# Kernel optimization log

Measured on AMD Instinct MI355X. Metric: run time of the kernel, lower is better.

Reference implementation:

```python
import jax, jax.numpy as jnp
import numpy as np

N_PL = 16      # PiecewiseLin resolution
OBJECTS = 10   # top-k objects kept / max count


def plin(w, x):
    """PiecewiseLin forward: w is [N_PL+1], x is any-shape tensor in [0,1]."""
    w = jnp.abs(w)
    w = w / w.sum()
    csum = jnp.cumsum(w)                     # [N_PL+1]
    y = N_PL * x
    idx = y.astype(jnp.int32)                # trunc toward zero (x >= 0)
    f = y - jnp.trunc(y)                     # fractional part
    lo = csum[jnp.minimum(idx, N_PL)]
    hi = w[jnp.minimum(idx + 1, N_PL)]
    return lo + f * hi


def _area(box):  # box: [n, 4, o]
    return jnp.clip(box[:, 2] - box[:, 0], 0.0, None) * jnp.clip(box[:, 3] - box[:, 1], 0.0, None)


def _iou(a, b):  # a, b: [n, 4, o] -> [n, o, o]
    mn = jnp.maximum(a[:, :2, :, None], b[:, :2, None, :])
    mx = jnp.minimum(a[:, 2:, :, None], b[:, 2:, None, :])
    wh = jnp.clip(mx - mn, 0.0, None)
    inter = wh[:, 0] * wh[:, 1]
    aa = _area(a)[:, :, None]
    ab = _area(b)[:, None, :]
    return inter / (aa + ab - inter + 1e-12)


def counter_forward(boxes, attention, ws):
    n = boxes.shape[0]
    # filter_most_important: top-k by attention
    att, idx = jax.lax.top_k(attention, OBJECTS)                       # [n, o]
    idx_b = jnp.broadcast_to(idx[:, None, :], (n, 4, OBJECTS))
    boxes = jnp.take_along_axis(boxes, idx_b, axis=2)                  # [n, 4, o]
    att = jax.nn.sigmoid(att)                                          # already_sigmoided=False

    relev = att[:, :, None] * att[:, None, :]                          # [n, o, o]
    dist = 1.0 - _iou(boxes, boxes)                                    # [n, o, o]

    score = plin(ws[0], relev) * plin(ws[1], dist)
    dedup = plin(ws[3], relev) * plin(ws[4], dist)

    # deduplicate
    att_diff = jnp.abs(att[:, :, None] - att[:, None, :])              # [n, o, o]
    score_diff = jnp.abs(dedup[..., :, None] - dedup[..., None, :])    # [n, o, o, o]
    sim = plin(ws[2], 1.0 - score_diff).prod(axis=1) * plin(ws[2], 1.0 - att_diff)  # [n, o, o]
    row_sims = sim.sum(axis=2)                                         # [n, o]
    all_sims = row_sims[:, :, None] * row_sims[:, None, :]             # [n, o, o]

    score = score / all_sims
    correction = plin(ws[0], att * att) / row_sims                     # [n, o]
    total = score.sum(axis=(1, 2))[:, None] + correction.sum(axis=1, keepdims=True)  # [n, 1]
    total = jnp.sqrt(total + 1e-20)

    # to_one_hot
    s = jnp.clip(total, 0.0, float(OBJECTS))                           # [n, 1]
    i = s.astype(jnp.int32)[:, 0]
    f = s - jnp.trunc(s)
    tl = jax.nn.one_hot(jnp.minimum(i, OBJECTS), OBJECTS + 1, dtype=s.dtype)
    tr = jax.nn.one_hot(jnp.minimum(i + 1, OBJECTS), OBJECTS + 1, dtype=s.dtype)
    one_hot = (1.0 - f) * tl + f * tr                                  # [n, o+1]

    # confidence
    att_conf = jnp.abs(plin(ws[5], att) - 0.5)                         # [n, o]
    dist_conf = jnp.abs(plin(ws[6], dist) - 0.5)                       # [n, o, o]
    conf = plin(ws[7], att_conf.mean(axis=1, keepdims=True)
                + dist_conf.mean(axis=2).mean(axis=1, keepdims=True))  # [n, 1]
    return one_hot * conf                                              # [n, o+1]


def setup_inputs() -> dict:
    key = jax.random.key(0)
    k1, k2, k3 = jax.random.split(key, 3)
    n, m = 32768, 36
    boxes = jax.random.uniform(k1, (n, 4, m), dtype=jnp.float32)
    attention = jax.random.normal(k2, (n, m), dtype=jnp.float32)
    ws = jax.random.uniform(k3, (8, N_PL + 1), dtype=jnp.float32, minval=0.1, maxval=1.0)
    return {"boxes": boxes, "attention": attention, "ws": ws}


def reference(boxes, attention, ws):
    return counter_forward(boxes, attention, ws)
```

## Files before the change

kernel.cpp:

```cpp
#include <hip/hip_runtime.h>
#include <math.h>

#define N_PL 16
#define NT   17
#define OBJ  10
#define M    36
#define SPB  4
#define BLK  64

#define R_ATT  0
#define R_X0   10
#define R_Y0   20
#define R_X1   30
#define R_Y1   40
#define R_AR   50
#define R_DED  60
#define R_SIM  160
#define R_RF   260
#define RSTRIDE 273

__constant__ unsigned char c_p55[55] = {
 0x00,0x01,0x02,0x03,0x04,0x05,0x06,0x07,0x08,0x09,
 0x11,0x12,0x13,0x14,0x15,0x16,0x17,0x18,0x19,
 0x22,0x23,0x24,0x25,0x26,0x27,0x28,0x29,
 0x33,0x34,0x35,0x36,0x37,0x38,0x39,
 0x44,0x45,0x46,0x47,0x48,0x49,
 0x55,0x56,0x57,0x58,0x59,
 0x66,0x67,0x68,0x69,
 0x77,0x78,0x79,
 0x88,0x89,
 0x99};
__constant__ unsigned char c_p45[45] = {
 0x01,0x02,0x03,0x04,0x05,0x06,0x07,0x08,0x09,
 0x12,0x13,0x14,0x15,0x16,0x17,0x18,0x19,
 0x23,0x24,0x25,0x26,0x27,0x28,0x29,
 0x34,0x35,0x36,0x37,0x38,0x39,
 0x45,0x46,0x47,0x48,0x49,
 0x56,0x57,0x58,0x59,
 0x67,0x68,0x69,
 0x78,0x79,
 0x89};

__device__ __forceinline__ float plin_tab(const float* s_tab, int t, float x) {
    const float* wn = s_tab + t * NT;
    const float* cs = s_tab + 136 + t * NT;
    float y = 16.0f * x;
    int idx = (int)y;
    float f = y - (float)idx;
    int i0 = idx < N_PL ? idx : N_PL;
    int i1 = (idx + 1) < N_PL ? (idx + 1) : N_PL;
    return __builtin_fmaf(f, wn[i1], cs[i0]);
}

__device__ __forceinline__ unsigned long long mkkey(float v, int m) {
    unsigned int b = __float_as_uint(v);
    unsigned int u = b ^ (0x80000000u | (unsigned int)((int)b >> 31));
    return ((unsigned long long)u << 6) | (unsigned int)(63 - m);
}

__global__ __launch_bounds__(BLK, 4) void counter_kernel(
    const float* __restrict__ boxes,
    const float* __restrict__ attn,
    const float* __restrict__ ws,
    float* __restrict__ out,
    int n)
{
    __shared__ float s_tab[272];
    __shared__ float s_reg[SPB * RSTRIDE];

    const int tid = threadIdx.x;
    const int g = tid & 15;
    const int p = tid >> 4;
    float* R = s_reg + p * RSTRIDE;

    if (tid < 8) {
        float w[NT]; float sum = 0.f;
        #pragma unroll
        for (int k = 0; k < NT; ++k) { w[k] = fabsf(ws[tid * NT + k]); sum += w[k]; }
        float rs = 1.f / sum;
        float c = 0.f;
        #pragma unroll
        for (int k = 0; k < NT; ++k) {
            float v = w[k] * rs;
            s_tab[tid * NT + k] = v;
            c += v;
            s_tab[136 + tid * NT + k] = c;
        }
    }

    int s = blockIdx.x * SPB + p;
    const bool active = (s < n);
    if (!active) s = n - 1;

    const float* arow = attn + (size_t)s * M;
    float mv[3]; unsigned long long myk[3];
    #pragma unroll
    for (int k = 0; k < 3; ++k) {
        int e = g + 16 * k;
        bool ok = e < M;
        float v = ok ? arow[e] : 0.f;
        mv[k] = v;
        myk[k] = ok ? mkkey(v, e) : 0ull;
    }
    int rnk0 = 0, rnk1 = 0, rnk2 = 0;
    #pragma unroll
    for (int c4 = 0; c4 < 9; ++c4) {
        float4 t4 = ((const float4*)arow)[c4];
        float vv[4] = {t4.x, t4.y, t4.z, t4.w};
        #pragma unroll
        for (int q = 0; q < 4; ++q) {
            unsigned long long kk = mkkey(vv[q], 4 * c4 + q);
            rnk0 += (kk > myk[0]) ? 1 : 0;
            rnk1 += (kk > myk[1]) ? 1 : 0;
            rnk2 += (kk > myk[2]) ? 1 : 0;
        }
    }
    int rnk[3] = {rnk0, rnk1, rnk2};

    __syncthreads();

    const float* brow = boxes + (size_t)s * (4 * M);
    float mA = 0.f;
    #pragma unroll
    for (int k = 0; k < 3; ++k) {
        int e = g + 16 * k;
        if (e < M && rnk[k] < OBJ) {
            float a = 1.f / (1.f + __expf(-mv[k]));
            int r = rnk[k];
            R[R_ATT + r] = a;
            mA += fabsf(plin_tab(s_tab, 5, a) - 0.5f);
            float x0 = brow[e], y0 = brow[M + e], x1 = brow[2 * M + e], y1 = brow[3 * M + e];
            R[R_X0 + r] = x0; R[R_Y0 + r] = y0;
            R[R_X1 + r] = x1; R[R_Y1 + r] = y1;
            R[R_AR + r] = fmaxf(x1 - x0, 0.f) * fmaxf(y1 - y0, 0.f);
        }
    }
    __syncthreads();

    float mD = 0.f;
    float sc_loc[4];
    #pragma unroll
    for (int t = 0; t < 4; ++t) {
        int q = g + 16 * t;
        bool act = (q < 55);
        int pk = c_p55[act ? q : 0];
        int i = pk >> 4, j = pk & 15;
        float wx = fminf(R[R_X1 + i], R[R_X1 + j]) - fmaxf(R[R_X0 + i], R[R_X0 + j]);
        float wy = fminf(R[R_Y1 + i], R[R_Y1 + j]) - fmaxf(R[R_Y0 + i], R[R_Y0 + j]);
        float inter = fmaxf(wx, 0.f) * fmaxf(wy, 0.f);
        float un = R[R_AR + i] + R[R_AR + j] - inter + 1e-12f;
        float d = 1.f - inter * __builtin_amdgcn_rcpf(un);
        float relev = R[R_ATT + i] * R[R_ATT + j];
        float dd = plin_tab(s_tab, 3, relev) * plin_tab(s_tab, 4, d);
        sc_loc[t] = plin_tab(s_tab, 0, relev) * plin_tab(s_tab, 1, d);
        float dc = fabsf(plin_tab(s_tab, 6, d) - 0.5f);
        if (act) {
            R[R_DED + i * OBJ + j] = dd;
            R[R_DED + j * OBJ + i] = dd;
            mD += (i != j) ? 2.f * dc : dc;
        }
    }
    __syncthreads();

    #pragma unroll
    for (int t = 0; t < 3; ++t) {
        int q = g + 16 * t;
        bool act = (q < 45);
        int pk = c_p45[act ? q : 0];
        int i = pk >> 4, j = pk & 15;
        float prod = plin_tab(s_tab, 2, 1.f - fabsf(R[R_ATT + i] - R[R_ATT + j]));
        #pragma unroll
        for (int a = 0; a < OBJ; ++a) {
            float da = fabsf(R[R_DED + a * OBJ + i] - R[R_DED + a * OBJ + j]);
            prod *= plin_tab(s_tab, 2, 1.f - da);
        }
        if (act) {
            R[R_SIM + i * OBJ + j] = prod;
            R[R_SIM + j * OBJ + i] = prod;
        }
    }
    __syncthreads();

    if (g < OBJ) {
        float c16 = s_tab[136 + 2 * NT + N_PL];
        float c2 = c16 * c16, c4 = c2 * c2, c8 = c4 * c4;
        float sum = c8 * c2 * c16;
        #pragma unroll
        for (int j = 0; j < OBJ; ++j)
            sum += (j == g) ? 0.f : R[R_SIM + g * OBJ + j];
        R[R_RF + g] = 1.f / sum;
    }
    __syncthreads();

    float tot = 0.f;
    #pragma unroll
    for (int t = 0; t < 4; ++t) {
        int q = g + 16 * t;
        bool act = (q < 55);
        int pk = c_p55[act ? q : 0];
        int i = pk >> 4, j = pk & 15;
        float term = sc_loc[t] * R[R_RF + i] * R[R_RF + j];
        if (act) tot += (i != j) ? 2.f * term : term;
    }
    if (g < OBJ) {
        float ai = R[R_ATT + g];
        tot += plin_tab(s_tab, 0, ai * ai) * R[R_RF + g];
    }
    float carg = mA * 0.1f + mD * 0.01f;
    tot  += __shfl_xor(tot, 1);  tot  += __shfl_xor(tot, 2);
    tot  += __shfl_xor(tot, 4);  tot  += __shfl_xor(tot, 8);
    carg += __shfl_xor(carg, 1); carg += __shfl_xor(carg, 2);
    carg += __shfl_xor(carg, 4); carg += __shfl_xor(carg, 8);

    float total = sqrtf(tot + 1e-20f);
    float conf = plin_tab(s_tab, 7, carg);
    float scl = fminf(fmaxf(total, 0.f), 10.f);
    int i0 = (int)scl;
    float f = scl - (float)i0;
    int lo = i0 < OBJ ? i0 : OBJ;
    int hi = (i0 + 1) < OBJ ? (i0 + 1) : OBJ;

    if (active && g <= OBJ) {
        float vv = ((g == lo) ? (1.f - f) : 0.f) + ((g == hi) ? f : 0.f);
        out[(size_t)s * (OBJ + 1) + g] = vv * conf;
    }
}

extern "C" void kernel_launch(void* const* d_in, const int* in_sizes, int n_in,
                              void* d_out, int out_size, void* d_ws, size_t ws_size,
                              hipStream_t stream) {
    const float* boxes = (const float*)d_in[0];
    const float* attn  = (const float*)d_in[1];
    const float* ws    = (const float*)d_in[2];
    float* out = (float*)d_out;
    int n = in_sizes[1] / M;
    int blocks = (n + SPB - 1) / SPB;
    hipLaunchKernelGGL(counter_kernel, dim3(blocks), dim3(BLK), 0, stream,
                       boxes, attn, ws, out, n);
}
```

Before: 87.11 us.

## Interleave plin tables and vectorize shared-memory layout for pair computations

Packs each PiecewiseLin table entry as a float2 of cumulative sum and next weight, so every lookup is one 8-byte LDS read instead of two scalar reads. Per-sample scratch is split into float4 box and float2 attention/area arrays, and the dedup and similarity matrices use a 12-float padded row stride, so rows load with float4/float2 vector reads. It also caches the pair index across loops and zeroes the similarity diagonal so row sums can be read without branches. This cuts LDS instruction count in the inner dedup-product loop, at the cost of more shared memory from the padding and possible bank conflicts on the wider accesses.

```diff
diff --git a/kernel.cpp b/kernel.cpp
--- a/kernel.cpp
+++ b/kernel.cpp
@@ -7,17 +7,7 @@
 #define M    36
 #define SPB  4
 #define BLK  64
-
-#define R_ATT  0
-#define R_X0   10
-#define R_Y0   20
-#define R_X1   30
-#define R_Y1   40
-#define R_AR   50
-#define R_DED  60
-#define R_SIM  160
-#define R_RF   260
-#define RSTRIDE 273
+#define CSTR 12
 
 __constant__ unsigned char c_p55[55] = {
  0x00,0x01,0x02,0x03,0x04,0x05,0x06,0x07,0x08,0x09,
@@ -41,15 +31,13 @@
  0x78,0x79,
  0x89};
 
-__device__ __forceinline__ float plin_tab(const float* s_tab, int t, float x) {
-    const float* wn = s_tab + t * NT;
-    const float* cs = s_tab + 136 + t * NT;
+__device__ __forceinline__ float plin2(const float2* tb, float x) {
     float y = 16.0f * x;
     int idx = (int)y;
     float f = y - (float)idx;
     int i0 = idx < N_PL ? idx : N_PL;
-    int i1 = (idx + 1) < N_PL ? (idx + 1) : N_PL;
-    return __builtin_fmaf(f, wn[i1], cs[i0]);
+    float2 cw = tb[i0];
+    return __builtin_fmaf(f, cw.y, cw.x);
 }
 
 __device__ __forceinline__ unsigned long long mkkey(float v, int m) {
@@ -65,26 +53,30 @@
     float* __restrict__ out,
     int n)
 {
-    __shared__ float s_tab[272];
-    __shared__ float s_reg[SPB * RSTRIDE];
+    __shared__ float2 s_tab2[8 * NT];
+    __shared__ float4 s_bx[SPB][OBJ];
+    __shared__ float2 s_aa[SPB][OBJ];
+    __shared__ float  s_ded[SPB][CSTR * OBJ];
+    __shared__ float  s_sim[SPB][CSTR * OBJ];
+    __shared__ float  s_rf[SPB][OBJ];
 
     const int tid = threadIdx.x;
     const int g = tid & 15;
     const int p = tid >> 4;
-    float* R = s_reg + p * RSTRIDE;
 
     if (tid < 8) {
         float w[NT]; float sum = 0.f;
         #pragma unroll
         for (int k = 0; k < NT; ++k) { w[k] = fabsf(ws[tid * NT + k]); sum += w[k]; }
         float rs = 1.f / sum;
+        float wn[NT];
+        #pragma unroll
+        for (int k = 0; k < NT; ++k) wn[k] = w[k] * rs;
         float c = 0.f;
         #pragma unroll
         for (int k = 0; k < NT; ++k) {
-            float v = w[k] * rs;
-            s_tab[tid * NT + k] = v;
-            c += v;
-            s_tab[136 + tid * NT + k] = c;
+            c += wn[k];
+            s_tab2[tid * NT + k] = make_float2(c, wn[k < N_PL ? k + 1 : N_PL]);
         }
     }
 
@@ -127,68 +119,89 @@
         if (e < M && rnk[k] < OBJ) {
             float a = 1.f / (1.f + __expf(-mv[k]));
             int r = rnk[k];
-            R[R_ATT + r] = a;
-            mA += fabsf(plin_tab(s_tab, 5, a) - 0.5f);
+            mA += fabsf(plin2(s_tab2 + 5 * NT, a) - 0.5f);
             float x0 = brow[e], y0 = brow[M + e], x1 = brow[2 * M + e], y1 = brow[3 * M + e];
-            R[R_X0 + r] = x0; R[R_Y0 + r] = y0;
-            R[R_X1 + r] = x1; R[R_Y1 + r] = y1;
-            R[R_AR + r] = fmaxf(x1 - x0, 0.f) * fmaxf(y1 - y0, 0.f);
+            s_bx[p][r] = make_float4(x0, y0, x1, y1);
+            s_aa[p][r] = make_float2(a, fmaxf(x1 - x0, 0.f) * fmaxf(y1 - y0, 0.f));
         }
     }
     __syncthreads();
 
     float mD = 0.f;
     float sc_loc[4];
+    int pkA[4];
     #pragma unroll
     for (int t = 0; t < 4; ++t) {
         int q = g + 16 * t;
         bool act = (q < 55);
         int pk = c_p55[act ? q : 0];
+        pkA[t] = pk;
         int i = pk >> 4, j = pk & 15;
-        float wx = fminf(R[R_X1 + i], R[R_X1 + j]) - fmaxf(R[R_X0 + i], R[R_X0 + j]);
-        float wy = fminf(R[R_Y1 + i], R[R_Y1 + j]) - fmaxf(R[R_Y0 + i], R[R_Y0 + j]);
+        float4 bi = s_bx[p][i], bj = s_bx[p][j];
+        float2 ai = s_aa[p][i], aj = s_aa[p][j];
+        float wx = fminf(bi.z, bj.z) - fmaxf(bi.x, bj.x);
+        float wy = fminf(bi.w, bj.w) - fmaxf(bi.y, bj.y);
         float inter = fmaxf(wx, 0.f) * fmaxf(wy, 0.f);
-        float un = R[R_AR + i] + R[R_AR + j] - inter + 1e-12f;
+        float un = ai.y + aj.y - inter + 1e-12f;
         float d = 1.f - inter * __builtin_amdgcn_rcpf(un);
-        float relev = R[R_ATT + i] * R[R_ATT + j];
-        float dd = plin_tab(s_tab, 3, relev) * plin_tab(s_tab, 4, d);
-        sc_loc[t] = plin_tab(s_tab, 0, relev) * plin_tab(s_tab, 1, d);
-        float dc = fabsf(plin_tab(s_tab, 6, d) - 0.5f);
+        float relev = ai.x * aj.x;
+        float dd = plin2(s_tab2 + 3 * NT, relev) * plin2(s_tab2 + 4 * NT, d);
+        sc_loc[t] = plin2(s_tab2 + 0 * NT, relev) * plin2(s_tab2 + 1 * NT, d);
+        float dc = fabsf(plin2(s_tab2 + 6 * NT, d) - 0.5f);
         if (act) {
-            R[R_DED + i * OBJ + j] = dd;
-            R[R_DED + j * OBJ + i] = dd;
+            s_ded[p][i * CSTR + j] = dd;
+            s_ded[p][j * CSTR + i] = dd;
             mD += (i != j) ? 2.f * dc : dc;
         }
     }
     __syncthreads();
 
+    if (g < OBJ) s_sim[p][g * CSTR + g] = 0.f;
     #pragma unroll
     for (int t = 0; t < 3; ++t) {
         int q = g + 16 * t;
         bool act = (q < 45);
         int pk = c_p45[act ? q : 0];
         int i = pk >> 4, j = pk & 15;
-        float prod = plin_tab(s_tab, 2, 1.f - fabsf(R[R_ATT + i] - R[R_ATT + j]));
-        #pragma unroll
-        for (int a = 0; a < OBJ; ++a) {
-            float da = fabsf(R[R_DED + a * OBJ + i] - R[R_DED + a * OBJ + j]);
-            prod *= plin_tab(s_tab, 2, 1.f - da);
-        }
+        float2 ai = s_aa[p][i], aj = s_aa[p][j];
+        float prod = plin2(s_tab2 + 2 * NT, 1.f - fabsf(ai.x - aj.x));
+        const float* ci = &s_ded[p][i * CSTR];
+        const float* cj = &s_ded[p][j * CSTR];
+        float4 ci0 = *(const float4*)ci;
+        float4 ci1 = *(const float4*)(ci + 4);
+        float2 ci2 = *(const float2*)(ci + 8);
+        float4 cj0 = *(const float4*)cj;
+        float4 cj1 = *(const float4*)(cj + 4);
+        float2 cj2 = *(const float2*)(cj + 8);
+        const float2* tb2 = s_tab2 + 2 * NT;
+        prod *= plin2(tb2, 1.f - fabsf(ci0.x - cj0.x));
+        prod *= plin2(tb2, 1.f - fabsf(ci0.y - cj0.y));
+        prod *= plin2(tb2, 1.f - fabsf(ci0.z - cj0.z));
+        prod *= plin2(tb2, 1.f - fabsf(ci0.w - cj0.w));
+        prod *= plin2(tb2, 1.f - fabsf(ci1.x - cj1.x));
+        prod *= plin2(tb2, 1.f - fabsf(ci1.y - cj1.y));
+        prod *= plin2(tb2, 1.f - fabsf(ci1.z - cj1.z));
+        prod *= plin2(tb2, 1.f - fabsf(ci1.w - cj1.w));
+        prod *= plin2(tb2, 1.f - fabsf(ci2.x - cj2.x));
+        prod *= plin2(tb2, 1.f - fabsf(ci2.y - cj2.y));
         if (act) {
-            R[R_SIM + i * OBJ + j] = prod;
-            R[R_SIM + j * OBJ + i] = prod;
+            s_sim[p][i * CSTR + j] = prod;
+            s_sim[p][j * CSTR + i] = prod;
         }
     }
     __syncthreads();
 
     if (g < OBJ) {
-        float c16 = s_tab[136 + 2 * NT + N_PL];
+        float c16 = s_tab2[2 * NT + N_PL].x;
         float c2 = c16 * c16, c4 = c2 * c2, c8 = c4 * c4;
-        float sum = c8 * c2 * c16;
-        #pragma unroll
-        for (int j = 0; j < OBJ; ++j)
-            sum += (j == g) ? 0.f : R[R_SIM + g * OBJ + j];
-        R[R_RF + g] = 1.f / sum;
+        float diag = c8 * c2 * c16;
+        const float* rw = &s_sim[p][g * CSTR];
+        float4 r0 = *(const float4*)rw;
+        float4 r1 = *(const float4*)(rw + 4);
+        float2 r2 = *(const float2*)(rw + 8);
+        float sum = diag + r0.x + r0.y + r0.z + r0.w
+                         + r1.x + r1.y + r1.z + r1.w + r2.x + r2.y;
+        s_rf[p][g] = 1.f / sum;
     }
     __syncthreads();
 
@@ -197,14 +210,14 @@
     for (int t = 0; t < 4; ++t) {
         int q = g + 16 * t;
         bool act = (q < 55);
-        int pk = c_p55[act ? q : 0];
+        int pk = pkA[t];
         int i = pk >> 4, j = pk & 15;
-        float term = sc_loc[t] * R[R_RF + i] * R[R_RF + j];
+        float term = sc_loc[t] * s_rf[p][i] * s_rf[p][j];
         if (act) tot += (i != j) ? 2.f * term : term;
     }
     if (g < OBJ) {
-        float ai = R[R_ATT + g];
-        tot += plin_tab(s_tab, 0, ai * ai) * R[R_RF + g];
+        float ai = s_aa[p][g].x;
+        tot += plin2(s_tab2 + 0 * NT, ai * ai) * s_rf[p][g];
     }
     float carg = mA * 0.1f + mD * 0.01f;
     tot  += __shfl_xor(tot, 1);  tot  += __shfl_xor(tot, 2);
@@ -213,7 +226,7 @@
     carg += __shfl_xor(carg, 4); carg += __shfl_xor(carg, 8);
 
     float total = sqrtf(tot + 1e-20f);
-    float conf = plin_tab(s_tab, 7, carg);
+    float conf = plin2(s_tab2 + 7 * NT, carg);
     float scl = fminf(fmaxf(total, 0.f), 10.f);
     int i0 = (int)scl;
     float f = scl - (float)i0;
```

After: 85.01 us (median of 2 runs). 2.4% less time.
